# Kernel tuning notes

Hardware: AMD Instinct MI355X
Metric: run time of the kernel (lower is better)

Reference implementation:

```python
import jax, jax.numpy as jnp
import numpy as np

B, C, N, K = 8, 96, 3136, 18
C1 = 1e-6
C2 = 1e-6


def _gather(x, idx):
    # x: [B, C, N], idx: [B, N, K] -> [B, C, N, K]
    return jax.vmap(lambda xb, ib: xb[:, ib])(x, idx)


def setup_inputs() -> dict:
    key = jax.random.key(0)
    k1, k2, k3 = jax.random.split(key, 3)
    x = jax.random.normal(k1, (B, C, N, 1), dtype=jnp.float32)
    x_p = jax.random.uniform(k2, (B, C, N, 1), dtype=jnp.float32)
    edge_index = jax.random.randint(k3, (2, B, N, K), 0, N, dtype=jnp.int32)
    return {"x": x, "x_p": x_p, "edge_index": edge_index}


def reference(x, x_p, edge_index):
    xs = x[..., 0]    # [B, C, N]
    xps = x_p[..., 0]  # [B, C, N]
    idx_i = edge_index[1]  # centers  [B, N, K]
    idx_j = edge_index[0]  # neighbors [B, N, K]

    x_i = _gather(xs, idx_i)   # [B, C, N, K]
    x_j = _gather(xs, idx_j)
    xp_i = _gather(xps, idx_i)
    xp_j = _gather(xps, idx_j)

    # SSIM-like statistics over the channel dim (axis=1)
    x_i_mean = jnp.mean(x_i, axis=1, keepdims=True)  # [B, 1, N, K]
    x_j_mean = jnp.mean(x_j, axis=1, keepdims=True)
    i_var = jnp.mean((x_i - x_i_mean) ** 2, axis=1, keepdims=True)
    j_var = jnp.mean((x_j - x_j_mean) ** 2, axis=1, keepdims=True)
    ij_covs = jnp.mean(x_i * x_j, axis=1, keepdims=True) - x_i_mean * x_j_mean

    S1 = (2.0 * x_i_mean * x_j_mean + C1) / (x_i_mean ** 2 + x_j_mean ** 2 + C1)
    S2 = (2.0 * ij_covs + C2) / (i_var + j_var + C2)
    sff = 1.0 - S1 * S2  # [B, 1, N, K]

    xps_ij = jnp.abs(xp_i - xp_j)              # [B, C, N, K]
    sum_xx = jnp.sum(xps_ij * sff, axis=-1)    # [B, C, N]
    sum_x = jnp.sum(xp_i, axis=-1) + jnp.sum(xp_j, axis=-1)
    Ex = sum_x + sum_xx                        # [B, C, N]
    return Ex[..., None]                       # [B, C, N, 1]
```

## Files before the change

kernel.cpp:

```cpp
#include <hip/hip_runtime.h>
#include <cstdint>
#include <cstddef>

constexpr int B = 8, C = 96, N = 3136, K = 18;
constexpr float C1c = 1e-6f, C2c = 1e-6f;

typedef unsigned int uint32;
typedef unsigned short ushort16;

__device__ inline float readlane_f(float v, int l) {
  return __builtin_bit_cast(float,
                            __builtin_amdgcn_readlane(__builtin_bit_cast(int, v), l));
}

__device__ inline ushort16 f2bf(float f) {
  uint32 u = __builtin_bit_cast(uint32, f);
  return (ushort16)((u + 0x7FFFu + ((u >> 16) & 1u)) >> 16);
}
__device__ inline float bflo(uint32 u) {
  return __builtin_bit_cast(float, u << 16);
}
__device__ inline float bfhi(uint32 u) {
  return __builtin_bit_cast(float, u & 0xFFFF0000u);
}
__device__ inline float dot2(uint32 a, uint32 b, float acc) {
  return fmaf(bflo(a), bflo(b), fmaf(bfhi(a), bfhi(b), acc));
}

__global__ __launch_bounds__(256) void fusedT_kernel(
    const float* __restrict__ x, const float* __restrict__ xp,
    ushort16* __restrict__ xT, ushort16* __restrict__ xpT,
    float2* __restrict__ cstat) {
  __shared__ float t0[C][33];
  __shared__ float t1[C][33];
  __shared__ float red1[8][33];
  __shared__ float red2[8][33];
  const int bid = blockIdx.x;
  const int b = bid & 7;
  const int n0 = (bid >> 3) * 32;
  const int tx = threadIdx.x & 31;
  const int ty = threadIdx.x >> 5;

  const float* xb = x + (size_t)b * C * N;
  const float* xpb = xp + (size_t)b * C * N;
  float s = 0.f, s2 = 0.f;
#pragma unroll
  for (int st = 0; st < 12; ++st) {
    const int c = st * 8 + ty;
    const float v = xb[(size_t)c * N + n0 + tx];
    const float u = xpb[(size_t)c * N + n0 + tx];
    t0[c][tx] = v;
    t1[c][tx] = u;
    s += v;
    s2 += v * v;
  }
  red1[ty][tx] = s;
  red2[ty][tx] = s2;
  __syncthreads();

  ushort16* xTb = xT + (size_t)b * N * C;
  ushort16* xpTb = xpT + (size_t)b * N * C;
  const int tid = threadIdx.x;
#pragma unroll
  for (int r = 0; r < 12; ++r) {
    const int f = r * 256 + tid;
    const int nl = f / 96;
    const int c = f - nl * 96;
    xTb[(size_t)(n0 + nl) * C + c] = f2bf(t0[c][nl]);
    xpTb[(size_t)(n0 + nl) * C + c] = f2bf(t1[c][nl]);
  }
  if (ty == 0) {
    float S = 0.f, S2 = 0.f;
#pragma unroll
    for (int yy = 0; yy < 8; ++yy) {
      S += red1[yy][tx];
      S2 += red2[yy][tx];
    }
    cstat[(size_t)b * N + n0 + tx] = make_float2(S, S2);
  }
}

__global__ __launch_bounds__(256, 4) void ssim_main_kernel(
    const ushort16* __restrict__ xT, const ushort16* __restrict__ xpT,
    const float2* __restrict__ cstat, const int* __restrict__ eidx,
    float* __restrict__ out) {
  const int wave = threadIdx.x >> 6;
  const int lane = threadIdx.x & 63;
  const int b = blockIdx.x & 7;
  const int tile = blockIdx.x >> 3;
  const int n = tile * 4 + wave;

  int myidx = 0;
  if (lane < 36) {
    const int s = (lane >= 18) ? 1 : 0;
    const int k = lane - 18 * s;
    myidx = eidx[((size_t)(s * B + b) * N + n) * K + k];
  }

  const ushort16* xb = xT + (size_t)b * N * C;
  const float2* cs = cstat + (size_t)b * N;
  const int g = lane >> 3;
  const int w = lane & 7;

  float sffr[3];
#pragma unroll
  for (int r = 0; r < 3; ++r) {
    int k = r * 8 + g;
    if (k > K - 1) k = K - 1;
    const int cj = __shfl(myidx, k, 64);
    const int ci = __shfl(myidx, 18 + k, 64);
    const uint2* xi = (const uint2*)(xb + (size_t)ci * C + 12 * w);
    const uint2* xj = (const uint2*)(xb + (size_t)cj * C + 12 * w);
    const uint2 a0 = xi[0], a1 = xi[1], a2 = xi[2];
    const uint2 q0 = xj[0], q1 = xj[1], q2 = xj[2];
    const float2 si = cs[ci];
    const float2 sj = cs[cj];

    float p = dot2(a0.x, q0.x, 0.f);
    p = dot2(a0.y, q0.y, p);
    p = dot2(a1.x, q1.x, p);
    p = dot2(a1.y, q1.y, p);
    p = dot2(a2.x, q2.x, p);
    p = dot2(a2.y, q2.y, p);
    p += __shfl_xor(p, 1, 64);
    p += __shfl_xor(p, 2, 64);
    p += __shfl_xor(p, 4, 64);

    const float mi = si.x * (1.0f / C), mj = sj.x * (1.0f / C);
    const float vi = si.y * (1.0f / C) - mi * mi;
    const float vj = sj.y * (1.0f / C) - mj * mj;
    const float cov = p * (1.0f / C) - mi * mj;
    const float S1 =
        (2.f * mi * mj + C1c) * __builtin_amdgcn_rcpf(mi * mi + mj * mj + C1c);
    const float S2 = (2.f * cov + C2c) * __builtin_amdgcn_rcpf(vi + vj + C2c);
    sffr[r] = 1.f - S1 * S2;
  }

  float sk[K];
#pragma unroll
  for (int k = 0; k < K; ++k) sk[k] = readlane_f(sffr[k >> 3], (k & 7) * 8);
  int jjs[K], jis[K];
#pragma unroll
  for (int k = 0; k < K; ++k) {
    jjs[k] = __builtin_amdgcn_readlane(myidx, k);
    jis[k] = __builtin_amdgcn_readlane(myidx, 18 + k);
  }

  const uint32* xpb32 = (const uint32*)(xpT + (size_t)b * N * C);
  const int l = (lane < 48) ? lane : 47;
  float tx = 0.f, ty = 0.f, ax = 0.f, ay = 0.f;
#pragma unroll
  for (int k = 0; k < K; ++k) {
    const uint32 a = xpb32[(size_t)jis[k] * 48 + l];
    const uint32 q = xpb32[(size_t)jjs[k] * 48 + l];
    const float a0 = bflo(a), a1 = bfhi(a);
    const float q0 = bflo(q), q1 = bfhi(q);
    tx += a0 + q0;
    ty += a1 + q1;
    ax = fmaf(fabsf(a0 - q0), sk[k], ax);
    ay = fmaf(fabsf(a1 - q1), sk[k], ay);
  }

  if (lane < 48) {
    float* ob = out + ((size_t)b * C + 2 * lane) * N + n;
    ob[0] = tx + ax;
    ob[N] = ty + ay;
  }
}

__global__ void fallback_kernel(const float* __restrict__ x,
                                const float* __restrict__ xp,
                                const int* __restrict__ e,
                                float* __restrict__ out) {
  const int gn = blockIdx.x * 64 + threadIdx.x;
  if (gn >= B * N) return;
  const int b = gn / N;
  const int n = gn - b * N;
  const float* xb = x + (size_t)b * C * N;
  const float* xpb = xp + (size_t)b * C * N;
  int ii[K], jj[K];
  float sff[K];
#pragma unroll
  for (int k = 0; k < K; ++k) {
    jj[k] = e[((size_t)(0 * B + b) * N + n) * K + k];
    ii[k] = e[((size_t)(1 * B + b) * N + n) * K + k];
    float si = 0, sj = 0, sii = 0, sjj = 0, sij = 0;
    for (int c = 0; c < C; ++c) {
      const float a = xb[(size_t)c * N + ii[k]];
      const float q = xb[(size_t)c * N + jj[k]];
      si += a; sj += q; sii += a * a; sjj += q * q; sij += a * q;
    }
    const float mi = si * (1.f / C), mj = sj * (1.f / C);
    const float vi = sii * (1.f / C) - mi * mi;
    const float vj = sjj * (1.f / C) - mj * mj;
    const float cov = sij * (1.f / C) - mi * mj;
    const float S1 = (2.f * mi * mj + C1c) / (mi * mi + mj * mj + C1c);
    const float S2 = (2.f * cov + C2c) / (vi + vj + C2c);
    sff[k] = 1.f - S1 * S2;
  }
  for (int c = 0; c < C; ++c) {
    float acc = 0.f;
#pragma unroll
    for (int k = 0; k < K; ++k) {
      const float a = xpb[(size_t)c * N + ii[k]];
      const float q = xpb[(size_t)c * N + jj[k]];
      acc += a + q + fabsf(a - q) * sff[k];
    }
    out[((size_t)b * C + c) * N + n] = acc;
  }
}

extern "C" void kernel_launch(void* const* d_in, const int* in_sizes, int n_in,
                              void* d_out, int out_size, void* d_ws, size_t ws_size,
                              hipStream_t stream) {
  const float* x = (const float*)d_in[0];
  const float* xp = (const float*)d_in[1];
  const int* e = (const int*)d_in[2];
  float* out = (float*)d_out;

  const size_t nBNC = (size_t)B * N * C;
  const size_t nBN = (size_t)B * N;
  const size_t need = 2 * nBNC * sizeof(ushort16) + nBN * sizeof(float2);

  if (ws_size >= need) {
    ushort16* xT = (ushort16*)d_ws;
    ushort16* xpT = xT + nBNC;
    float2* cstat = (float2*)(xpT + nBNC);

    fusedT_kernel<<<8 * (N / 32), 256, 0, stream>>>(x, xp, xT, xpT, cstat);
    ssim_main_kernel<<<(B * N) / 4, 256, 0, stream>>>(xT, xpT, cstat, e, out);
  } else {
    fallback_kernel<<<(B * N + 63) / 64, 64, 0, stream>>>(x, xp, e, out);
  }
}
```

Measured before the change: 41.88 us.

## Switch staging to fp16 with packed dot2 math and coalesce output via LDS

Transposed x and x_p are now stored as fp16 instead of bf16. The covariance dot product uses the hardware fdot2 instruction, and the neighbor accumulation uses packed half2 adds and FMAs spread over four partial accumulators. Outputs are staged through shared memory so each block writes 4 consecutive n per channel instead of scattered single-float stores. The intent is fewer ALU instructions and better store coalescing, at the cost of fp16 range and precision in the accumulations and an added block barrier.

```diff
diff --git a/kernel.cpp b/kernel.cpp
--- a/kernel.cpp
+++ b/kernel.cpp
@@ -7,24 +7,22 @@
 
 typedef unsigned int uint32;
 typedef unsigned short ushort16;
+typedef _Float16 h2 __attribute__((ext_vector_type(2)));
 
 __device__ inline float readlane_f(float v, int l) {
   return __builtin_bit_cast(float,
                             __builtin_amdgcn_readlane(__builtin_bit_cast(int, v), l));
 }
 
-__device__ inline ushort16 f2bf(float f) {
-  uint32 u = __builtin_bit_cast(uint32, f);
-  return (ushort16)((u + 0x7FFFu + ((u >> 16) & 1u)) >> 16);
-}
-__device__ inline float bflo(uint32 u) {
-  return __builtin_bit_cast(float, u << 16);
-}
-__device__ inline float bfhi(uint32 u) {
-  return __builtin_bit_cast(float, u & 0xFFFF0000u);
-}
-__device__ inline float dot2(uint32 a, uint32 b, float acc) {
-  return fmaf(bflo(a), bflo(b), fmaf(bfhi(a), bfhi(b), acc));
+__device__ inline ushort16 f2h(float f) {
+  return __builtin_bit_cast(ushort16, (_Float16)f);
+}
+__device__ inline h2 u2h2(uint32 u) { return __builtin_bit_cast(h2, u); }
+__device__ inline h2 habs2(h2 v) {
+  return __builtin_bit_cast(h2, __builtin_bit_cast(uint32, v) & 0x7FFF7FFFu);
+}
+__device__ inline float2 h22f2(h2 v) {
+  return make_float2((float)v.x, (float)v.y);
 }
 
 __global__ __launch_bounds__(256) void fusedT_kernel(
@@ -66,8 +64,8 @@
     const int f = r * 256 + tid;
     const int nl = f / 96;
     const int c = f - nl * 96;
-    xTb[(size_t)(n0 + nl) * C + c] = f2bf(t0[c][nl]);
-    xpTb[(size_t)(n0 + nl) * C + c] = f2bf(t1[c][nl]);
+    xTb[(size_t)(n0 + nl) * C + c] = f2h(t0[c][nl]);
+    xpTb[(size_t)(n0 + nl) * C + c] = f2h(t1[c][nl]);
   }
   if (ty == 0) {
     float S = 0.f, S2 = 0.f;
@@ -84,6 +82,7 @@
     const ushort16* __restrict__ xT, const ushort16* __restrict__ xpT,
     const float2* __restrict__ cstat, const int* __restrict__ eidx,
     float* __restrict__ out) {
+  __shared__ float ored[4][100];
   const int wave = threadIdx.x >> 6;
   const int lane = threadIdx.x & 63;
   const int b = blockIdx.x & 7;
@@ -116,12 +115,12 @@
     const float2 si = cs[ci];
     const float2 sj = cs[cj];
 
-    float p = dot2(a0.x, q0.x, 0.f);
-    p = dot2(a0.y, q0.y, p);
-    p = dot2(a1.x, q1.x, p);
-    p = dot2(a1.y, q1.y, p);
-    p = dot2(a2.x, q2.x, p);
-    p = dot2(a2.y, q2.y, p);
+    float p = __builtin_amdgcn_fdot2(u2h2(a0.x), u2h2(q0.x), 0.f, false);
+    p = __builtin_amdgcn_fdot2(u2h2(a0.y), u2h2(q0.y), p, false);
+    p = __builtin_amdgcn_fdot2(u2h2(a1.x), u2h2(q1.x), p, false);
+    p = __builtin_amdgcn_fdot2(u2h2(a1.y), u2h2(q1.y), p, false);
+    p = __builtin_amdgcn_fdot2(u2h2(a2.x), u2h2(q2.x), p, false);
+    p = __builtin_amdgcn_fdot2(u2h2(a2.y), u2h2(q2.y), p, false);
     p += __shfl_xor(p, 1, 64);
     p += __shfl_xor(p, 2, 64);
     p += __shfl_xor(p, 4, 64);
@@ -136,9 +135,6 @@
     sffr[r] = 1.f - S1 * S2;
   }
 
-  float sk[K];
-#pragma unroll
-  for (int k = 0; k < K; ++k) sk[k] = readlane_f(sffr[k >> 3], (k & 7) * 8);
   int jjs[K], jis[K];
 #pragma unroll
   for (int k = 0; k < K; ++k) {
@@ -148,23 +144,40 @@
 
   const uint32* xpb32 = (const uint32*)(xpT + (size_t)b * N * C);
   const int l = (lane < 48) ? lane : 47;
-  float tx = 0.f, ty = 0.f, ax = 0.f, ay = 0.f;
+  h2 accT[4] = {h2{0, 0}, h2{0, 0}, h2{0, 0}, h2{0, 0}};
+  h2 accX[4] = {h2{0, 0}, h2{0, 0}, h2{0, 0}, h2{0, 0}};
 #pragma unroll
   for (int k = 0; k < K; ++k) {
-    const uint32 a = xpb32[(size_t)jis[k] * 48 + l];
-    const uint32 q = xpb32[(size_t)jjs[k] * 48 + l];
-    const float a0 = bflo(a), a1 = bfhi(a);
-    const float q0 = bflo(q), q1 = bfhi(q);
-    tx += a0 + q0;
-    ty += a1 + q1;
-    ax = fmaf(fabsf(a0 - q0), sk[k], ax);
-    ay = fmaf(fabsf(a1 - q1), sk[k], ay);
-  }
+    const float sf = readlane_f(sffr[k >> 3], (k & 7) * 8);
+    const _Float16 sh = (_Float16)sf;
+    const h2 sf2 = h2{sh, sh};
+    const h2 a = u2h2(xpb32[(size_t)jis[k] * 48 + l]);
+    const h2 q = u2h2(xpb32[(size_t)jjs[k] * 48 + l]);
+    accT[k & 3] = accT[k & 3] + (a + q);
+    accX[k & 3] = habs2(a - q) * sf2 + accX[k & 3];
+  }
+  const float2 t0 = h22f2(accT[0]), t1 = h22f2(accT[1]);
+  const float2 t2 = h22f2(accT[2]), t3 = h22f2(accT[3]);
+  const float2 x0 = h22f2(accX[0]), x1 = h22f2(accX[1]);
+  const float2 x2 = h22f2(accX[2]), x3 = h22f2(accX[3]);
+  const float resx = (t0.x + t1.x) + (t2.x + t3.x) + (x0.x + x1.x) + (x2.x + x3.x);
+  const float resy = (t0.y + t1.y) + (t2.y + t3.y) + (x0.y + x1.y) + (x2.y + x3.y);
 
   if (lane < 48) {
-    float* ob = out + ((size_t)b * C + 2 * lane) * N + n;
-    ob[0] = tx + ax;
-    ob[N] = ty + ay;
+    ored[wave][2 * lane] = resx;
+    ored[wave][2 * lane + 1] = resy;
+  }
+  __syncthreads();
+  const int n0 = tile * 4;
+  const int tid = threadIdx.x;
+  {
+    const int ch = tid >> 2, nn = tid & 3;
+    out[((size_t)b * C + ch) * N + n0 + nn] = ored[nn][ch];
+  }
+  if (tid < 128) {
+    const int t2i = 256 + tid;
+    const int ch = t2i >> 2, nn = t2i & 3;
+    out[((size_t)b * C + ch) * N + n0 + nn] = ored[nn][ch];
   }
 }
 
```

Result: faster. 36.38 us, median of 2 (-13.1%).
